# Performance work log

Measured on AMD Instinct MI355X. Metric: run time of the kernel, lower is better.

The kernel has to match this reference:

```python
import jax, jax.numpy as jnp
import numpy as np

N_LAYERS, H, D, DH = 4, 16, 1024, 64
V_FR, V_EN = 32000, 32000
L_FR, L_EN, B = 513, 512, 2


def _pos_enc(x):
    # x: [L, B, D]; pe[i,j] = sin(i/10000^(j/D)) if j even else cos(i/10000^((j-1)/D))
    L, _, D_ = x.shape
    pos = jnp.arange(L, dtype=jnp.float32)[:, None]
    j = jnp.arange(D_)
    ang = pos / jnp.power(10000.0, (j - (j % 2)).astype(jnp.float32) / D_)
    pe = jnp.where(j % 2 == 0, jnp.sin(ang), jnp.cos(ang))
    return x + pe[:, None, :]


def _ln(x, g, b):
    mu = jnp.mean(x, -1, keepdims=True)
    var = jnp.mean((x - mu) ** 2, -1, keepdims=True)
    return (x - mu) * jax.lax.rsqrt(var + 1e-5) * g + b


def _mha(q_in, k_in, v_in, w, bias, causal):
    # w: [3, H, D, dh], bias: [3, H, dh]
    dh = w.shape[-1]
    Q = jnp.einsum('bld,hde->bhle', q_in, w[0]) + bias[0][None, :, None, :]
    K = jnp.einsum('bmd,hde->bhme', k_in, w[1]) + bias[1][None, :, None, :]
    V = jnp.einsum('bmd,hde->bhme', v_in, w[2]) + bias[2][None, :, None, :]
    s = jnp.einsum('bhle,bhme->bhlm', Q, K) / jnp.sqrt(jnp.float32(dh))
    if causal:
        m = jnp.tril(jnp.ones((s.shape[-2], s.shape[-1]), bool))
        s = jnp.where(m, s, -jnp.inf)
    a = jax.nn.softmax(s, axis=-1)
    o = jnp.einsum('bhlm,bhme->bhle', a, V)
    b_, h_, l_, dh_ = o.shape
    return o.transpose(0, 2, 1, 3).reshape(b_, l_, h_ * dh_)


def setup_inputs() -> dict:
    key = jax.random.key(0)
    ks = jax.random.split(key, 24)
    s = 0.02
    rn = lambda k, shp: jax.random.normal(k, shp, jnp.float32) * s
    return {
        'fr': jax.random.randint(ks[0], (L_FR, B), 0, V_FR),
        'en': jax.random.randint(ks[1], (L_EN, B), 0, V_EN),
        'emb_fr': rn(ks[2], (V_FR, D)),
        'emb_en': rn(ks[3], (V_EN, D)),
        'enc_qkv_w': rn(ks[4], (N_LAYERS, 3, H, D, DH)),
        'enc_qkv_b': rn(ks[5], (N_LAYERS, 3, H, DH)),
        'enc_fc1_w': rn(ks[6], (N_LAYERS, D, D)),
        'enc_fc1_b': rn(ks[7], (N_LAYERS, D)),
        'enc_fc2_w': rn(ks[8], (N_LAYERS, D, D)),
        'enc_fc2_b': rn(ks[9], (N_LAYERS, D)),
        'enc_ln_g': jnp.ones((N_LAYERS, 2, D)) + rn(ks[10], (N_LAYERS, 2, D)),
        'enc_ln_b': rn(ks[11], (N_LAYERS, 2, D)),
        'dec_self_qkv_w': rn(ks[12], (N_LAYERS, 3, H, D, DH)),
        'dec_self_qkv_b': rn(ks[13], (N_LAYERS, 3, H, DH)),
        'dec_cross_qkv_w': rn(ks[14], (N_LAYERS, 3, H, D, DH)),
        'dec_cross_qkv_b': rn(ks[15], (N_LAYERS, 3, H, DH)),
        'dec_fc1_w': rn(ks[16], (N_LAYERS, D, D)),
        'dec_fc1_b': rn(ks[17], (N_LAYERS, D)),
        'dec_fc2_w': rn(ks[18], (N_LAYERS, D, D)),
        'dec_fc2_b': rn(ks[19], (N_LAYERS, D)),
        'dec_ln_g': jnp.ones((N_LAYERS, 3, D)) + rn(ks[20], (N_LAYERS, 3, D)),
        'dec_ln_b': rn(ks[21], (N_LAYERS, 3, D)),
        'out_w': rn(ks[22], (D, V_EN)),
        'out_b': rn(ks[23], (V_EN,)),
    }


def reference(fr, en, emb_fr, emb_en, enc_qkv_w, enc_qkv_b, enc_fc1_w, enc_fc1_b,
              enc_fc2_w, enc_fc2_b, enc_ln_g, enc_ln_b, dec_self_qkv_w,
              dec_self_qkv_b, dec_cross_qkv_w, dec_cross_qkv_b, dec_fc1_w,
              dec_fc1_b, dec_fc2_w, dec_fc2_b, dec_ln_g, dec_ln_b, out_w, out_b):
    # Encoder (dropout p=0 -> identity in eval math)
    x = _pos_enc(emb_fr[fr[1:]]).transpose(1, 0, 2)  # [B, L_src, D]
    for n in range(N_LAYERS):
        a = _mha(x, x, x, enc_qkv_w[n], enc_qkv_b[n], causal=False)
        x = _ln(x + a, enc_ln_g[n, 0], enc_ln_b[n, 0])
        h = jnp.maximum(x @ enc_fc1_w[n] + enc_fc1_b[n], 0.0) @ enc_fc2_w[n] + enc_fc2_b[n]
        x = _ln(x + h, enc_ln_g[n, 1], enc_ln_b[n, 1])
    enc_out = x
    # Decoder
    y = _pos_enc(emb_en[en]).transpose(1, 0, 2)  # [B, L_tgt, D]
    for n in range(N_LAYERS):
        a = _mha(y, y, y, dec_self_qkv_w[n], dec_self_qkv_b[n], causal=True)
        y = _ln(y + a, dec_ln_g[n, 0], dec_ln_b[n, 0])
        c = _mha(y, enc_out, enc_out, dec_cross_qkv_w[n], dec_cross_qkv_b[n], causal=False)
        y = _ln(y + c, dec_ln_g[n, 1], dec_ln_b[n, 1])
        h = jnp.maximum(y @ dec_fc1_w[n] + dec_fc1_b[n], 0.0) @ dec_fc2_w[n] + dec_fc2_b[n]
        y = _ln(y + h, dec_ln_g[n, 2], dec_ln_b[n, 2])
    return y @ out_w + out_b  # [B, L_tgt, V_EN]
```

## Files before the change

### kernel.cpp

```cpp
#include <hip/hip_runtime.h>
#include <stdint.h>
#include <stddef.h>

typedef unsigned short u16;
typedef __attribute__((ext_vector_type(8))) short bf16x8;
typedef __attribute__((ext_vector_type(4))) float f32x4;

#define DEV __device__ __forceinline__

DEV float b2f(u16 u) { union { float f; uint32_t i; } v; v.i = ((uint32_t)u) << 16; return v.f; }
DEV u16 f2b(float f) {
  uint32_t x = __float_as_uint(f);
  x += 0x7fffu + ((x >> 16) & 1u);
  return (u16)(x >> 16);
}
DEV bf16x8 ld8f(const float* f) {
  float4 a = *(const float4*)f;
  float4 b = *(const float4*)(f + 4);
  bf16x8 r;
  ((u16*)&r)[0] = f2b(a.x); ((u16*)&r)[1] = f2b(a.y);
  ((u16*)&r)[2] = f2b(a.z); ((u16*)&r)[3] = f2b(a.w);
  ((u16*)&r)[4] = f2b(b.x); ((u16*)&r)[5] = f2b(b.y);
  ((u16*)&r)[6] = f2b(b.z); ((u16*)&r)[7] = f2b(b.w);
  return r;
}
DEV void gload16(const u16* g, u16* l) {
  __builtin_amdgcn_global_load_lds((const __attribute__((address_space(1))) void*)g,
                                   (__attribute__((address_space(3))) void*)l, 16, 0, 0);
}
DEV f32x4 mfma16(bf16x8 a, bf16x8 b, f32x4 c) {
  return __builtin_amdgcn_mfma_f32_16x16x32_bf16(a, b, c, 0, 0, 0);
}

__global__ __launch_bounds__(256) void transpose_w(const float* __restrict__ src,
                                                   u16* __restrict__ dst, int K, int N) {
  __shared__ u16 t[32][33];
  int tx = threadIdx.x, ty = threadIdx.y;
  int k0 = blockIdx.x * 32, n0 = blockIdx.y * 32;
  size_t base = (size_t)blockIdx.z * K * N;
#pragma unroll
  for (int i = 0; i < 4; i++) {
    int k = ty + 8 * i;
    t[k][tx] = f2b(src[base + (size_t)(k0 + k) * N + n0 + tx]);
  }
  __syncthreads();
#pragma unroll
  for (int i = 0; i < 4; i++) {
    int n = ty + 8 * i;
    dst[base + (size_t)(n0 + n) * K + k0 + tx] = t[tx][n];
  }
}

__global__ __launch_bounds__(256) void embed_k(const int* __restrict__ tok, const float* __restrict__ emb,
                                               float* __restrict__ o32, u16* __restrict__ ob, int shift) {
  int row = blockIdx.x;
  int b = row >> 9, l = row & 511;
  int tk = tok[(size_t)(l + shift) * 2 + b];
  const float* e = emb + (size_t)tk * 1024;
  const float c0 = -9.210340371976184f / 1024.f;
#pragma unroll
  for (int i = 0; i < 4; i++) {
    int d = threadIdx.x + i * 256;
    int j2 = d & ~1;
    float ang = (float)l * expf(c0 * (float)j2);
    float pe = (d & 1) ? cosf(ang) : sinf(ang);
    float rv = e[d] + pe;
    o32[(size_t)row * 1024 + d] = rv;
    ob[(size_t)row * 1024 + d] = f2b(rv);
  }
}

__global__ __launch_bounds__(256) void ln_k(const float* a, const float* d,
                                            const float* __restrict__ g, const float* __restrict__ bb,
                                            float* o32, u16* __restrict__ ob) {
  int row = blockIdx.x;
  int tid = threadIdx.x;
  const float* ar = a + (size_t)row * 1024;
  const float* dr = d + (size_t)row * 1024;
  float v[4];
  float s = 0.f, s2 = 0.f;
#pragma unroll
  for (int i = 0; i < 4; i++) {
    float tv = ar[tid + 256 * i] + dr[tid + 256 * i];
    v[i] = tv; s += tv; s2 += tv * tv;
  }
#pragma unroll
  for (int off = 1; off < 64; off <<= 1) {
    s += __shfl_xor(s, off);
    s2 += __shfl_xor(s2, off);
  }
  __shared__ float red[8];
  int wid = tid >> 6;
  if ((tid & 63) == 0) { red[wid * 2] = s; red[wid * 2 + 1] = s2; }
  __syncthreads();
  s = red[0] + red[2] + red[4] + red[6];
  s2 = red[1] + red[3] + red[5] + red[7];
  float mu = s * (1.f / 1024.f);
  float var = s2 * (1.f / 1024.f) - mu * mu;
  float inv = rsqrtf(var + 1e-5f);
#pragma unroll
  for (int i = 0; i < 4; i++) {
    int c = tid + 256 * i;
    float ov = (v[i] - mu) * inv * g[c] + bb[c];
    o32[(size_t)row * 1024 + c] = ov;
    ob[(size_t)row * 1024 + c] = f2b(ov);
  }
}

template <int BM, int BN, bool RELU, bool OUT32, bool SWZ>
__global__ __launch_bounds__(256) void gemm_tile(const u16* __restrict__ A, const u16* __restrict__ BT,
                                                 const float* __restrict__ bias, void* __restrict__ out,
                                                 int N, int K) {
  constexpr int FM = BM / 32, FN = BN / 32;
  __shared__ __align__(16) u16 lA[BM * 32];
  __shared__ __align__(16) u16 lB[BN * 32];
  int bx, by;
  if (SWZ) {
    int b = blockIdx.x;
    int p = (b & 7) + 8 * (b >> 6);
    if (p >= N / BN) return;
    bx = p;
    by = (b >> 3) & 7;
  } else {
    bx = blockIdx.x;
    by = blockIdx.y;
  }
  int tid = threadIdx.x, lane = tid & 63, wid = tid >> 6;
  int l15 = lane & 15, lg = lane >> 4;
  int bm = by * BM, bn = bx * BN;
  int wr = (wid >> 1) * (BM / 2), wc = (wid & 1) * (BN / 2);
  f32x4 acc[FM][FN] = {};
  int r_s = tid >> 2, c_s = tid & 3;
  for (int kt = 0; kt < K; kt += 32) {
    __syncthreads();
#pragma unroll
    for (int i = 0; i < BM / 64; i++)
      gload16(A + (size_t)(bm + i * 64 + r_s) * K + kt + c_s * 8, &lA[(size_t)(i * 256 + wid * 64) * 8]);
#pragma unroll
    for (int i = 0; i < BN / 64; i++)
      gload16(BT + (size_t)(bn + i * 64 + r_s) * K + kt + c_s * 8, &lB[(size_t)(i * 256 + wid * 64) * 8]);
    __syncthreads();
    bf16x8 af[FM], bf_[FN];
#pragma unroll
    for (int m = 0; m < FM; m++) af[m] = *(const bf16x8*)&lA[(wr + m * 16 + l15) * 32 + lg * 8];
#pragma unroll
    for (int n = 0; n < FN; n++) bf_[n] = *(const bf16x8*)&lB[(wc + n * 16 + l15) * 32 + lg * 8];
#pragma unroll
    for (int m = 0; m < FM; m++)
#pragma unroll
      for (int n = 0; n < FN; n++) acc[m][n] = mfma16(af[m], bf_[n], acc[m][n]);
  }
#pragma unroll
  for (int n = 0; n < FN; n++) {
    int col = bn + wc + n * 16 + l15;
    float bv = bias[col];
#pragma unroll
    for (int m = 0; m < FM; m++) {
#pragma unroll
      for (int r = 0; r < 4; r++) {
        int row = bm + wr + m * 16 + lg * 4 + r;
        float v = acc[m][n][r] + bv;
        if (RELU) v = fmaxf(v, 0.f);
        if (OUT32) ((float*)out)[(size_t)row * N + col] = v;
        else ((u16*)out)[(size_t)row * N + col] = f2b(v);
      }
    }
  }
}

__global__ __launch_bounds__(256) void gemm_qkv2(const u16* __restrict__ Aq, const u16* __restrict__ Akv,
                                                 const u16* __restrict__ WT, const float* __restrict__ bias,
                                                 u16* __restrict__ Qo, u16* __restrict__ Ko,
                                                 u16* __restrict__ Vto) {
  __shared__ __align__(16) u16 lA[64 * 32];
  __shared__ __align__(16) u16 lB[64 * 32];
  int bx = blockIdx.x, by = blockIdx.y;
  int t = bx >> 4;
  const u16* A = (t == 0) ? Aq : Akv;
  int tid = threadIdx.x, lane = tid & 63, wid = tid >> 6;
  int l15 = lane & 15, lg = lane >> 4;
  int bm = by * 64, bn = bx * 64;
  int wr = (wid >> 1) * 32, wc = (wid & 1) * 32;
  f32x4 acc[2][2] = {};
  int r_s = tid >> 2, c_s = tid & 3;
  for (int kt = 0; kt < 1024; kt += 32) {
    __syncthreads();
    gload16(A + (size_t)(bm + r_s) * 1024 + kt + c_s * 8, &lA[(size_t)(wid * 64) * 8]);
    gload16(WT + (size_t)(bn + r_s) * 1024 + kt + c_s * 8, &lB[(size_t)(wid * 64) * 8]);
    __syncthreads();
    bf16x8 af[2], bf_[2];
#pragma unroll
    for (int m = 0; m < 2; m++) af[m] = *(const bf16x8*)&lA[(wr + m * 16 + l15) * 32 + lg * 8];
#pragma unroll
    for (int n = 0; n < 2; n++) bf_[n] = *(const bf16x8*)&lB[(wc + n * 16 + l15) * 32 + lg * 8];
#pragma unroll
    for (int m = 0; m < 2; m++)
#pragma unroll
      for (int n = 0; n < 2; n++) acc[m][n] = mfma16(af[m], bf_[n], acc[m][n]);
  }
#pragma unroll
  for (int n = 0; n < 2; n++) {
    int col = bn + wc + n * 16 + l15;
    int h = (col >> 6) & 15, e = col & 63;
    float bv = bias[col];
#pragma unroll
    for (int m = 0; m < 2; m++) {
#pragma unroll
      for (int r = 0; r < 4; r++) {
        int row = bm + wr + m * 16 + lg * 4 + r;
        int b = row >> 9, l = row & 511;
        u16 vbv = f2b(acc[m][n][r] + bv);
        size_t bhead = (size_t)b * 16 + h;
        if (t == 0) Qo[(bhead * 512 + l) * 64 + e] = vbv;
        else if (t == 1) Ko[(bhead * 512 + l) * 64 + e] = vbv;
        else Vto[(bhead * 64 + e) * 512 + l] = vbv;
      }
    }
  }
}

__global__ __launch_bounds__(256) void gemm_bn(const u16* __restrict__ A, const float* __restrict__ B,
                                               const float* __restrict__ bias, float* __restrict__ out,
                                               int N, int K) {
  __shared__ __align__(16) u16 lA[128 * 32];
  __shared__ __align__(16) u16 lBn[32 * 128];
  int b = blockIdx.x;
  int p = (b & 7) + 8 * (b >> 6);
  if (p >= N / 128) return;
  int by = (b >> 3) & 7;
  int tid = threadIdx.x, lane = tid & 63;
  int wid = tid >> 6;
  int l15 = lane & 15, lg = lane >> 4;
  int bm = by * 128, bn = p * 128;
  int wr = (wid >> 1) * 64, wc = (wid & 1) * 64;
  f32x4 acc[4][4] = {};
  int r_s = tid >> 2, c_s = tid & 3;
  int br = tid >> 4, bc = tid & 15;
  for (int kt = 0; kt < K; kt += 32) {
    bf16x8 va[2], vb[2];
#pragma unroll
    for (int it = 0; it < 2; it++) {
      va[it] = *(const bf16x8*)&A[(size_t)(bm + it * 64 + r_s) * K + kt + c_s * 8];
      vb[it] = ld8f(B + (size_t)(kt + it * 16 + br) * N + bn + bc * 8);
    }
    __syncthreads();
#pragma unroll
    for (int it = 0; it < 2; it++) {
      *(bf16x8*)&lA[(size_t)(it * 256 + tid) * 8] = va[it];
      *(bf16x8*)&lBn[(size_t)(it * 256 + tid) * 8] = vb[it];
    }
    __syncthreads();
    bf16x8 af[4], bfr[4];
#pragma unroll
    for (int m = 0; m < 4; m++) af[m] = *(const bf16x8*)&lA[(wr + m * 16 + l15) * 32 + lg * 8];
#pragma unroll
    for (int n = 0; n < 4; n++) {
#pragma unroll
      for (int j = 0; j < 8; j++)
        ((short*)&bfr[n])[j] = (short)lBn[(lg * 8 + j) * 128 + wc + n * 16 + l15];
    }
#pragma unroll
    for (int m = 0; m < 4; m++)
#pragma unroll
      for (int n = 0; n < 4; n++) acc[m][n] = mfma16(af[m], bfr[n], acc[m][n]);
  }
#pragma unroll
  for (int n = 0; n < 4; n++) {
    int col = bn + wc + n * 16 + l15;
    float bv = bias[col];
#pragma unroll
    for (int m = 0; m < 4; m++) {
#pragma unroll
      for (int r = 0; r < 4; r++) {
        int row = bm + wr + m * 16 + lg * 4 + r;
        out[(size_t)row * N + col] = acc[m][n][r] + bv;
      }
    }
  }
}

template <bool CAUSAL>
__global__ __launch_bounds__(256) void attn_k(const u16* __restrict__ Qb, const u16* __restrict__ Kb,
                                              const u16* __restrict__ Vtb, float* __restrict__ Ob) {
  int bh = blockIdx.y;
  int tid = threadIdx.x, lane = tid & 63, w = tid >> 6;
  int l15 = lane & 15, lg = lane >> 4;
  int q0 = blockIdx.x * 64 + w * 16;
  const u16* Qh = Qb + (size_t)bh * 512 * 64;
  const u16* Kh = Kb + (size_t)bh * 512 * 64;
  const u16* Vh = Vtb + (size_t)bh * 64 * 512;
  __shared__ __align__(16) u16 P[4][16 * 40];
  u16* Pw = &P[w][0];
  bf16x8 qa0 = *(const bf16x8*)&Qh[(size_t)(q0 + l15) * 64 + lg * 8];
  bf16x8 qa1 = *(const bf16x8*)&Qh[(size_t)(q0 + l15) * 64 + 32 + lg * 8];
  f32x4 acc[4];
#pragma unroll
  for (int c = 0; c < 4; c++) acc[c] = (f32x4){0.f, 0.f, 0.f, 0.f};
  float mx_[4], ls[4];
#pragma unroll
  for (int r = 0; r < 4; r++) { mx_[r] = -1e30f; ls[r] = 0.f; }
  int ktend = CAUSAL ? ((q0 + 15) >> 5) : 15;
  for (int kt = 0; kt <= ktend; kt++) {
    int kv = kt * 32;
    f32x4 z = (f32x4){0.f, 0.f, 0.f, 0.f};
    bf16x8 k00 = *(const bf16x8*)&Kh[(size_t)(kv + l15) * 64 + lg * 8];
    bf16x8 k01 = *(const bf16x8*)&Kh[(size_t)(kv + l15) * 64 + 32 + lg * 8];
    f32x4 s0 = mfma16(qa0, k00, z);
    s0 = mfma16(qa1, k01, s0);
    bf16x8 k10 = *(const bf16x8*)&Kh[(size_t)(kv + 16 + l15) * 64 + lg * 8];
    bf16x8 k11 = *(const bf16x8*)&Kh[(size_t)(kv + 16 + l15) * 64 + 32 + lg * 8];
    f32x4 s1 = mfma16(qa0, k10, z);
    s1 = mfma16(qa1, k11, s1);
    float scn[4];
#pragma unroll
    for (int r = 0; r < 4; r++) {
      float a0 = s0[r] * 0.125f, a1 = s1[r] * 0.125f;
      if (CAUSAL) {
        int rowg = q0 + lg * 4 + r;
        if (kv + l15 > rowg) a0 = -1e30f;
        if (kv + 16 + l15 > rowg) a1 = -1e30f;
      }
      float mx = fmaxf(a0, a1);
#pragma unroll
      for (int off = 1; off < 16; off <<= 1) mx = fmaxf(mx, __shfl_xor(mx, off));
      float mn = fmaxf(mx_[r], mx);
      float sc = __expf(mx_[r] - mn);
      mx_[r] = mn;
      float p0 = __expf(a0 - mn), p1 = __expf(a1 - mn);
      float rs = p0 + p1;
#pragma unroll
      for (int off = 1; off < 16; off <<= 1) rs += __shfl_xor(rs, off);
      ls[r] = ls[r] * sc + rs;
      scn[r] = sc;
      int prow = lg * 4 + r;
      Pw[prow * 40 + l15] = f2b(p0);
      Pw[prow * 40 + 16 + l15] = f2b(p1);
    }
#pragma unroll
    for (int c = 0; c < 4; c++)
#pragma unroll
      for (int r = 0; r < 4; r++) acc[c][r] *= scn[r];
    bf16x8 pa = *(const bf16x8*)&Pw[l15 * 40 + lg * 8];
#pragma unroll
    for (int c = 0; c < 4; c++) {
      bf16x8 vb = *(const bf16x8*)&Vh[(size_t)(c * 16 + l15) * 512 + kv + lg * 8];
      acc[c] = mfma16(pa, vb, acc[c]);
    }
  }
  int b = bh >> 4, h = bh & 15;
#pragma unroll
  for (int r = 0; r < 4; r++) {
    float inv = 1.f / ls[r];
    int rowg = q0 + lg * 4 + r;
    float* orow = Ob + (size_t)(b * 512 + rowg) * 1024 + h * 64;
#pragma unroll
    for (int c = 0; c < 4; c++) orow[c * 16 + l15] = acc[c][r] * inv;
  }
}

extern "C" void kernel_launch(void* const* d_in, const int* in_sizes, int n_in,
                              void* d_out, int out_size, void* d_ws, size_t ws_size,
                              hipStream_t stream) {
  const int* fr = (const int*)d_in[0];
  const int* en = (const int*)d_in[1];
  const float* emb_fr = (const float*)d_in[2];
  const float* emb_en = (const float*)d_in[3];
  const float* enc_qkv_w = (const float*)d_in[4];
  const float* enc_qkv_b = (const float*)d_in[5];
  const float* enc_fc1_w = (const float*)d_in[6];
  const float* enc_fc1_b = (const float*)d_in[7];
  const float* enc_fc2_w = (const float*)d_in[8];
  const float* enc_fc2_b = (const float*)d_in[9];
  const float* enc_ln_g = (const float*)d_in[10];
  const float* enc_ln_bb = (const float*)d_in[11];
  const float* dec_self_qkv_w = (const float*)d_in[12];
  const float* dec_self_qkv_b = (const float*)d_in[13];
  const float* dec_cross_qkv_w = (const float*)d_in[14];
  const float* dec_cross_qkv_b = (const float*)d_in[15];
  const float* dec_fc1_w = (const float*)d_in[16];
  const float* dec_fc1_b = (const float*)d_in[17];
  const float* dec_fc2_w = (const float*)d_in[18];
  const float* dec_fc2_b = (const float*)d_in[19];
  const float* dec_ln_g = (const float*)d_in[20];
  const float* dec_ln_bb = (const float*)d_in[21];
  const float* out_w = (const float*)d_in[22];
  const float* out_b = (const float*)d_in[23];

  char* o8 = (char*)d_out;
  u16* qkvT_d = (u16*)o8;
  u16* fcT_d = (u16*)(o8 + 6291456);
  float* x32 = (float*)(o8 + 8388608);
  float* y32 = (float*)(o8 + 12582912);
  float* d32 = (float*)(o8 + 16777216);
  u16* xb = (u16*)(o8 + 20971520);
  u16* hb = (u16*)(o8 + 23068672);
  u16* Qb = (u16*)(o8 + 25165824);
  u16* Kb = (u16*)(o8 + 27262976);
  u16* Vtb = (u16*)(o8 + 29360128);

  char* w8 = (char*)d_ws;
  u16* yb = (u16*)w8;
  u16* outwT = (u16*)(w8 + 2097152);
  u16* eqkvT = (u16*)(w8 + 67633152);
  u16* dsqkvT = (u16*)(w8 + 92798976);
  u16* dcqkvT = (u16*)(w8 + 117964800);
  u16* efc1T = (u16*)(w8 + 143130624);
  u16* efc2T = (u16*)(w8 + 151519232);
  u16* dfc1T = (u16*)(w8 + 159907840);
  u16* dfc2T = (u16*)(w8 + 168296448);
  int tier = (ws_size >= 176685056u) ? 2 : (ws_size >= 67633152u) ? 1 : 0;

  dim3 tb(32, 8);
  if (tier >= 1)
    transpose_w<<<dim3(32, 1000, 1), tb, 0, stream>>>(out_w, outwT, 1024, 32000);
  if (tier == 2) {
    transpose_w<<<dim3(32, 2, 192), tb, 0, stream>>>(enc_qkv_w, eqkvT, 1024, 64);
    transpose_w<<<dim3(32, 2, 192), tb, 0, stream>>>(dec_self_qkv_w, dsqkvT, 1024, 64);
    transpose_w<<<dim3(32, 2, 192), tb, 0, stream>>>(dec_cross_qkv_w, dcqkvT, 1024, 64);
    transpose_w<<<dim3(32, 32, 4), tb, 0, stream>>>(enc_fc1_w, efc1T, 1024, 1024);
    transpose_w<<<dim3(32, 32, 4), tb, 0, stream>>>(enc_fc2_w, efc2T, 1024, 1024);
    transpose_w<<<dim3(32, 32, 4), tb, 0, stream>>>(dec_fc1_w, dfc1T, 1024, 1024);
    transpose_w<<<dim3(32, 32, 4), tb, 0, stream>>>(dec_fc2_w, dfc2T, 1024, 1024);
  }

  embed_k<<<1024, 256, 0, stream>>>(fr, emb_fr, x32, xb, 1);
  embed_k<<<1024, 256, 0, stream>>>(en, emb_en, y32, yb, 0);

  for (int n = 0; n < 4; n++) {
    const u16* wqkv;
    if (tier == 2) wqkv = eqkvT + (size_t)n * 3145728;
    else {
      transpose_w<<<dim3(32, 2, 48), tb, 0, stream>>>(enc_qkv_w + (size_t)n * 48 * 65536, qkvT_d, 1024, 64);
      wqkv = qkvT_d;
    }
    gemm_qkv2<<<dim3(48, 16), 256, 0, stream>>>(xb, xb, wqkv, enc_qkv_b + (size_t)n * 3072, Qb, Kb, Vtb);
    attn_k<false><<<dim3(8, 32), 256, 0, stream>>>(Qb, Kb, Vtb, d32);
    ln_k<<<1024, 256, 0, stream>>>(x32, d32, enc_ln_g + (size_t)(n * 2) * 1024,
                                   enc_ln_bb + (size_t)(n * 2) * 1024, x32, xb);
    const u16* w1;
    if (tier == 2) w1 = efc1T + (size_t)n * 1048576;
    else {
      transpose_w<<<dim3(32, 32, 1), tb, 0, stream>>>(enc_fc1_w + (size_t)n * 1048576, fcT_d, 1024, 1024);
      w1 = fcT_d;
    }
    gemm_tile<64, 64, true, false, false><<<dim3(16, 16), 256, 0, stream>>>(
        xb, w1, enc_fc1_b + (size_t)n * 1024, hb, 1024, 1024);
    const u16* w2;
    if (tier == 2) w2 = efc2T + (size_t)n * 1048576;
    else {
      transpose_w<<<dim3(32, 32, 1), tb, 0, stream>>>(enc_fc2_w + (size_t)n * 1048576, fcT_d, 1024, 1024);
      w2 = fcT_d;
    }
    gemm_tile<64, 64, false, true, false><<<dim3(16, 16), 256, 0, stream>>>(
        hb, w2, enc_fc2_b + (size_t)n * 1024, d32, 1024, 1024);
    ln_k<<<1024, 256, 0, stream>>>(x32, d32, enc_ln_g + (size_t)(n * 2 + 1) * 1024,
                                   enc_ln_bb + (size_t)(n * 2 + 1) * 1024, x32, xb);
  }
  for (int n = 0; n < 4; n++) {
    const u16* wq;
    if (tier == 2) wq = dsqkvT + (size_t)n * 3145728;
    else {
      transpose_w<<<dim3(32, 2, 48), tb, 0, stream>>>(dec_self_qkv_w + (size_t)n * 48 * 65536, qkvT_d, 1024, 64);
      wq = qkvT_d;
    }
    gemm_qkv2<<<dim3(48, 16), 256, 0, stream>>>(yb, yb, wq, dec_self_qkv_b + (size_t)n * 3072, Qb, Kb, Vtb);
    attn_k<true><<<dim3(8, 32), 256, 0, stream>>>(Qb, Kb, Vtb, d32);
    ln_k<<<1024, 256, 0, stream>>>(y32, d32, dec_ln_g + (size_t)(n * 3) * 1024,
                                   dec_ln_bb + (size_t)(n * 3) * 1024, y32, yb);
    if (tier == 2) wq = dcqkvT + (size_t)n * 3145728;
    else {
      transpose_w<<<dim3(32, 2, 48), tb, 0, stream>>>(dec_cross_qkv_w + (size_t)n * 48 * 65536, qkvT_d, 1024, 64);
      wq = qkvT_d;
    }
    gemm_qkv2<<<dim3(48, 16), 256, 0, stream>>>(yb, xb, wq, dec_cross_qkv_b + (size_t)n * 3072, Qb, Kb, Vtb);
    attn_k<false><<<dim3(8, 32), 256, 0, stream>>>(Qb, Kb, Vtb, d32);
    ln_k<<<1024, 256, 0, stream>>>(y32, d32, dec_ln_g + (size_t)(n * 3 + 1) * 1024,
                                   dec_ln_bb + (size_t)(n * 3 + 1) * 1024, y32, yb);
    const u16* w1;
    if (tier == 2) w1 = dfc1T + (size_t)n * 1048576;
    else {
      transpose_w<<<dim3(32, 32, 1), tb, 0, stream>>>(dec_fc1_w + (size_t)n * 1048576, fcT_d, 1024, 1024);
      w1 = fcT_d;
    }
    gemm_tile<64, 64, true, false, false><<<dim3(16, 16), 256, 0, stream>>>(
        yb, w1, dec_fc1_b + (size_t)n * 1024, hb, 1024, 1024);
    const u16* w2;
    if (tier == 2) w2 = dfc2T + (size_t)n * 1048576;
    else {
      transpose_w<<<dim3(32, 32, 1), tb, 0, stream>>>(dec_fc2_w + (size_t)n * 1048576, fcT_d, 1024, 1024);
      w2 = fcT_d;
    }
    gemm_tile<64, 64, false, true, false><<<dim3(16, 16), 256, 0, stream>>>(
        hb, w2, dec_fc2_b + (size_t)n * 1024, d32, 1024, 1024);
    ln_k<<<1024, 256, 0, stream>>>(y32, d32, dec_ln_g + (size_t)(n * 3 + 2) * 1024,
                                   dec_ln_bb + (size_t)(n * 3 + 2) * 1024, y32, yb);
  }
  if (tier >= 1)
    gemm_tile<128, 128, false, true, true><<<dim3(2048), 256, 0, stream>>>(
        yb, outwT, out_b, (float*)d_out, 32000, 1024);
  else
    gemm_bn<<<dim3(2048), 256, 0, stream>>>(yb, out_w, out_b, (float*)d_out, 32000, 1024);
}
```

Measured before the change: 1.055 ms.

## Triple-buffer LDS in GEMM kernels with async prefetch two stages ahead

The tiled GEMM and QKV projection kernels move from a single LDS buffer with two barriers per K-step to a three-stage ring. Global-to-LDS loads are issued two tiles ahead, and explicit vmcnt waits plus a single s_barrier per iteration replace the syncthreads pairs. The aim is to overlap global memory latency with MFMA work. It triples LDS use, which could lower occupancy, and the hand-written waitcnt counts must match the number of loads in flight for correctness.

```diff
diff --git a/kernel.cpp b/kernel.cpp
--- a/kernel.cpp
+++ b/kernel.cpp
@@ -108,12 +108,13 @@
 }
 
 template <int BM, int BN, bool RELU, bool OUT32, bool SWZ>
-__global__ __launch_bounds__(256) void gemm_tile(const u16* __restrict__ A, const u16* __restrict__ BT,
-                                                 const float* __restrict__ bias, void* __restrict__ out,
-                                                 int N, int K) {
+__global__ __launch_bounds__(256) void gemm_p3(const u16* __restrict__ A, const u16* __restrict__ BT,
+                                               const float* __restrict__ bias, void* __restrict__ out,
+                                               int N, int K) {
   constexpr int FM = BM / 32, FN = BN / 32;
-  __shared__ __align__(16) u16 lA[BM * 32];
-  __shared__ __align__(16) u16 lB[BN * 32];
+  constexpr int L = BM / 64 + BN / 64;
+  __shared__ __align__(16) u16 lA[3][BM * 32];
+  __shared__ __align__(16) u16 lB[3][BN * 32];
   int bx, by;
   if (SWZ) {
     int b = blockIdx.x;
@@ -131,24 +132,38 @@
   int wr = (wid >> 1) * (BM / 2), wc = (wid & 1) * (BN / 2);
   f32x4 acc[FM][FN] = {};
   int r_s = tid >> 2, c_s = tid & 3;
-  for (int kt = 0; kt < K; kt += 32) {
-    __syncthreads();
+  auto stage = [&](int buf, int kt) {
 #pragma unroll
     for (int i = 0; i < BM / 64; i++)
-      gload16(A + (size_t)(bm + i * 64 + r_s) * K + kt + c_s * 8, &lA[(size_t)(i * 256 + wid * 64) * 8]);
+      gload16(A + (size_t)(bm + i * 64 + r_s) * K + kt + c_s * 8, &lA[buf][(i * 256 + wid * 64) * 8]);
 #pragma unroll
     for (int i = 0; i < BN / 64; i++)
-      gload16(BT + (size_t)(bn + i * 64 + r_s) * K + kt + c_s * 8, &lB[(size_t)(i * 256 + wid * 64) * 8]);
-    __syncthreads();
+      gload16(BT + (size_t)(bn + i * 64 + r_s) * K + kt + c_s * 8, &lB[buf][(i * 256 + wid * 64) * 8]);
+  };
+  int nt = K >> 5;
+  stage(0, 0);
+  stage(1, 32);
+  asm volatile("s_waitcnt vmcnt(%0)" ::"n"(L) : "memory");
+  __builtin_amdgcn_s_barrier();
+  int cur = 0;
+  for (int t = 0; t < nt; t++) {
+    if (t + 2 < nt) stage(cur == 0 ? 2 : cur - 1, (t + 2) * 32);
     bf16x8 af[FM], bf_[FN];
 #pragma unroll
-    for (int m = 0; m < FM; m++) af[m] = *(const bf16x8*)&lA[(wr + m * 16 + l15) * 32 + lg * 8];
-#pragma unroll
-    for (int n = 0; n < FN; n++) bf_[n] = *(const bf16x8*)&lB[(wc + n * 16 + l15) * 32 + lg * 8];
+    for (int m = 0; m < FM; m++) af[m] = *(const bf16x8*)&lA[cur][(wr + m * 16 + l15) * 32 + lg * 8];
+#pragma unroll
+    for (int n = 0; n < FN; n++) bf_[n] = *(const bf16x8*)&lB[cur][(wc + n * 16 + l15) * 32 + lg * 8];
 #pragma unroll
     for (int m = 0; m < FM; m++)
 #pragma unroll
       for (int n = 0; n < FN; n++) acc[m][n] = mfma16(af[m], bf_[n], acc[m][n]);
+    if (t + 2 < nt) {
+      asm volatile("s_waitcnt vmcnt(%0)" ::"n"(L) : "memory");
+    } else if (t + 1 < nt) {
+      asm volatile("s_waitcnt vmcnt(0)" ::: "memory");
+    }
+    if (t + 1 < nt) __builtin_amdgcn_s_barrier();
+    cur = (cur == 2) ? 0 : cur + 1;
   }
 #pragma unroll
   for (int n = 0; n < FN; n++) {
@@ -168,35 +183,48 @@
   }
 }
 
-__global__ __launch_bounds__(256) void gemm_qkv2(const u16* __restrict__ Aq, const u16* __restrict__ Akv,
+__global__ __launch_bounds__(256) void gemm_qkv3(const u16* __restrict__ Aq, const u16* __restrict__ Akv,
                                                  const u16* __restrict__ WT, const float* __restrict__ bias,
                                                  u16* __restrict__ Qo, u16* __restrict__ Ko,
                                                  u16* __restrict__ Vto) {
-  __shared__ __align__(16) u16 lA[64 * 32];
-  __shared__ __align__(16) u16 lB[64 * 32];
+  __shared__ __align__(16) u16 lA[3][64 * 32];
+  __shared__ __align__(16) u16 lB[3][64 * 32];
   int bx = blockIdx.x, by = blockIdx.y;
-  int t = bx >> 4;
-  const u16* A = (t == 0) ? Aq : Akv;
+  int tsel = bx >> 4;
+  const u16* A = (tsel == 0) ? Aq : Akv;
   int tid = threadIdx.x, lane = tid & 63, wid = tid >> 6;
   int l15 = lane & 15, lg = lane >> 4;
   int bm = by * 64, bn = bx * 64;
   int wr = (wid >> 1) * 32, wc = (wid & 1) * 32;
   f32x4 acc[2][2] = {};
   int r_s = tid >> 2, c_s = tid & 3;
-  for (int kt = 0; kt < 1024; kt += 32) {
-    __syncthreads();
-    gload16(A + (size_t)(bm + r_s) * 1024 + kt + c_s * 8, &lA[(size_t)(wid * 64) * 8]);
-    gload16(WT + (size_t)(bn + r_s) * 1024 + kt + c_s * 8, &lB[(size_t)(wid * 64) * 8]);
-    __syncthreads();
+  auto stage = [&](int buf, int kt) {
+    gload16(A + (size_t)(bm + r_s) * 1024 + kt + c_s * 8, &lA[buf][(wid * 64) * 8]);
+    gload16(WT + (size_t)(bn + r_s) * 1024 + kt + c_s * 8, &lB[buf][(wid * 64) * 8]);
+  };
+  stage(0, 0);
+  stage(1, 32);
+  asm volatile("s_waitcnt vmcnt(2)" ::: "memory");
+  __builtin_amdgcn_s_barrier();
+  int cur = 0;
+  for (int t = 0; t < 32; t++) {
+    if (t + 2 < 32) stage(cur == 0 ? 2 : cur - 1, (t + 2) * 32);
     bf16x8 af[2], bf_[2];
 #pragma unroll
-    for (int m = 0; m < 2; m++) af[m] = *(const bf16x8*)&lA[(wr + m * 16 + l15) * 32 + lg * 8];
-#pragma unroll
-    for (int n = 0; n < 2; n++) bf_[n] = *(const bf16x8*)&lB[(wc + n * 16 + l15) * 32 + lg * 8];
+    for (int m = 0; m < 2; m++) af[m] = *(const bf16x8*)&lA[cur][(wr + m * 16 + l15) * 32 + lg * 8];
+#pragma unroll
+    for (int n = 0; n < 2; n++) bf_[n] = *(const bf16x8*)&lB[cur][(wc + n * 16 + l15) * 32 + lg * 8];
 #pragma unroll
     for (int m = 0; m < 2; m++)
 #pragma unroll
       for (int n = 0; n < 2; n++) acc[m][n] = mfma16(af[m], bf_[n], acc[m][n]);
+    if (t + 2 < 32) {
+      asm volatile("s_waitcnt vmcnt(2)" ::: "memory");
+    } else if (t + 1 < 32) {
+      asm volatile("s_waitcnt vmcnt(0)" ::: "memory");
+    }
+    if (t + 1 < 32) __builtin_amdgcn_s_barrier();
+    cur = (cur == 2) ? 0 : cur + 1;
   }
 #pragma unroll
   for (int n = 0; n < 2; n++) {
@@ -211,8 +239,8 @@
         int b = row >> 9, l = row & 511;
         u16 vbv = f2b(acc[m][n][r] + bv);
         size_t bhead = (size_t)b * 16 + h;
-        if (t == 0) Qo[(bhead * 512 + l) * 64 + e] = vbv;
-        else if (t == 1) Ko[(bhead * 512 + l) * 64 + e] = vbv;
+        if (tsel == 0) Qo[(bhead * 512 + l) * 64 + e] = vbv;
+        else if (tsel == 1) Ko[(bhead * 512 + l) * 64 + e] = vbv;
         else Vto[(bhead * 64 + e) * 512 + l] = vbv;
       }
     }
@@ -433,7 +461,7 @@
       transpose_w<<<dim3(32, 2, 48), tb, 0, stream>>>(enc_qkv_w + (size_t)n * 48 * 65536, qkvT_d, 1024, 64);
       wqkv = qkvT_d;
     }
-    gemm_qkv2<<<dim3(48, 16), 256, 0, stream>>>(xb, xb, wqkv, enc_qkv_b + (size_t)n * 3072, Qb, Kb, Vtb);
+    gemm_qkv3<<<dim3(48, 16), 256, 0, stream>>>(xb, xb, wqkv, enc_qkv_b + (size_t)n * 3072, Qb, Kb, Vtb);
     attn_k<false><<<dim3(8, 32), 256, 0, stream>>>(Qb, Kb, Vtb, d32);
     ln_k<<<1024, 256, 0, stream>>>(x32, d32, enc_ln_g + (size_t)(n * 2) * 1024,
                                    enc_ln_bb + (size_t)(n * 2) * 1024, x32, xb);
@@ -443,7 +471,7 @@
       transpose_w<<<dim3(32, 32, 1), tb, 0, stream>>>(enc_fc1_w + (size_t)n * 1048576, fcT_d, 1024, 1024);
       w1 = fcT_d;
     }
-    gemm_tile<64, 64, true, false, false><<<dim3(16, 16), 256, 0, stream>>>(
+    gemm_p3<64, 64, true, false, false><<<dim3(16, 16), 256, 0, stream>>>(
         xb, w1, enc_fc1_b + (size_t)n * 1024, hb, 1024, 1024);
     const u16* w2;
     if (tier == 2) w2 = efc2T + (size_t)n * 1048576;
@@ -451,7 +479,7 @@
       transpose_w<<<dim3(32, 32, 1), tb, 0, stream>>>(enc_fc2_w + (size_t)n * 1048576, fcT_d, 1024, 1024);
       w2 = fcT_d;
     }
-    gemm_tile<64, 64, false, true, false><<<dim3(16, 16), 256, 0, stream>>>(
+    gemm_p3<64, 64, false, true, false><<<dim3(16, 16), 256, 0, stream>>>(
         hb, w2, enc_fc2_b + (size_t)n * 1024, d32, 1024, 1024);
     ln_k<<<1024, 256, 0, stream>>>(x32, d32, enc_ln_g + (size_t)(n * 2 + 1) * 1024,
                                    enc_ln_bb + (size_t)(n * 2 + 1) * 1024, x32, xb);
@@ -463,7 +491,7 @@
       transpose_w<<<dim3(32, 2, 48), tb, 0, stream>>>(dec_self_qkv_w + (size_t)n * 48 * 65536, qkvT_d, 1024, 64);
       wq = qkvT_d;
     }
-    gemm_qkv2<<<dim3(48, 16), 256, 0, stream>>>(yb, yb, wq, dec_self_qkv_b + (size_t)n * 3072, Qb, Kb, Vtb);
+    gemm_qkv3<<<dim3(48, 16), 256, 0, stream>>>(yb, yb, wq, dec_self_qkv_b + (size_t)n * 3072, Qb, Kb, Vtb);
     attn_k<true><<<dim3(8, 32), 256, 0, stream>>>(Qb, Kb, Vtb, d32);
     ln_k<<<1024, 256, 0, stream>>>(y32, d32, dec_ln_g + (size_t)(n * 3) * 1024,
                                    dec_ln_bb + (size_t)(n * 3) * 1024, y32, yb);
@@ -472,7 +500,7 @@
       transpose_w<<<dim3(32, 2, 48), tb, 0, stream>>>(dec_cross_qkv_w + (size_t)n * 48 * 65536, qkvT_d, 1024, 64);
       wq = qkvT_d;
     }
-    gemm_qkv2<<<dim3(48, 16), 256, 0, stream>>>(yb, xb, wq, dec_cross_qkv_b + (size_t)n * 3072, Qb, Kb, Vtb);
+    gemm_qkv3<<<dim3(48, 16), 256, 0, stream>>>(yb, xb, wq, dec_cross_qkv_b + (size_t)n * 3072, Qb, Kb, Vtb);
     attn_k<false><<<dim3(8, 32), 256, 0, stream>>>(Qb, Kb, Vtb, d32);
     ln_k<<<1024, 256, 0, stream>>>(y32, d32, dec_ln_g + (size_t)(n * 3 + 1) * 1024,
                                    dec_ln_bb + (size_t)(n * 3 + 1) * 1024, y32, yb);
@@ -482,7 +510,7 @@
       transpose_w<<<dim3(32, 32, 1), tb, 0, stream>>>(dec_fc1_w + (size_t)n * 1048576, fcT_d, 1024, 1024);
       w1 = fcT_d;
     }
-    gemm_tile<64, 64, true, false, false><<<dim3(16, 16), 256, 0, stream>>>(
+    gemm_p3<64, 64, true, false, false><<<dim3(16, 16), 256, 0, stream>>>(
         yb, w1, dec_fc1_b + (size_t)n * 1024, hb, 1024, 1024);
     const u16* w2;
     if (tier == 2) w2 = dfc2T + (size_t)n * 1048576;
@@ -490,13 +518,13 @@
       transpose_w<<<dim3(32, 32, 1), tb, 0, stream>>>(dec_fc2_w + (size_t)n * 1048576, fcT_d, 1024, 1024);
       w2 = fcT_d;
     }
-    gemm_tile<64, 64, false, true, false><<<dim3(16, 16), 256, 0, stream>>>(
+    gemm_p3<64, 64, false, true, false><<<dim3(16, 16), 256, 0, stream>>>(
         hb, w2, dec_fc2_b + (size_t)n * 1024, d32, 1024, 1024);
     ln_k<<<1024, 256, 0, stream>>>(y32, d32, dec_ln_g + (size_t)(n * 3 + 2) * 1024,
                                    dec_ln_bb + (size_t)(n * 3 + 2) * 1024, y32, yb);
   }
   if (tier >= 1)
-    gemm_tile<128, 128, false, true, true><<<dim3(2048), 256, 0, stream>>>(
+    gemm_p3<128, 128, false, true, true><<<dim3(2048), 256, 0, stream>>>(
         yb, outwT, out_b, (float*)d_out, 32000, 1024);
   else
     gemm_bn<<<dim3(2048), 256, 0, stream>>>(yb, out_w, out_b, (float*)d_out, 32000, 1024);
```

Result: slower. 1.110 ms (+5.2%).
